# Performance work log

Measured on AMD Instinct MI355X. Metric: run time of the kernel, lower is better.

## Reference

```python
import jax, jax.numpy as jnp
import numpy as np

K = 3      # kernel size (hardcoded 3x3 in the torch module via repeat(...,9,...))
PAD = 1
STRIDE = 1


def _unfold(x):
    # torch.nn.functional.unfold equivalent: (B,C,H,W) -> (B,C,K,K,oh,ow)
    B, C, H, W = x.shape
    p = jax.lax.conv_general_dilated_patches(
        x, (K, K), (STRIDE, STRIDE), ((PAD, PAD), (PAD, PAD)))
    oh, ow = p.shape[2], p.shape[3]
    return p.reshape(B, C, K, K, oh, ow)


def setup_inputs() -> dict:
    key = jax.random.key(0)
    k1, k2, k3, k4 = jax.random.split(key, 4)
    B, Cin, Cout, H, W = 4, 64, 64, 128, 128
    inputs = jax.random.normal(k1, (B, Cin, H, W), jnp.float32)
    depth = jax.random.uniform(k2, (B, 1, H, W), jnp.float32)  # positive depths
    weight = jax.random.uniform(k3, (K, Cout, Cin, K, K), jnp.float32, minval=-0.05, maxval=0.05)
    bias = jax.random.uniform(k4, (Cout,), jnp.float32, minval=-0.05, maxval=0.05)
    return {"inputs": inputs, "depth": depth, "weight": weight, "bias": bias, "f": 1}


def reference(inputs, depth, weight, bias, f):
    # --- DepthKernelFn: per-depth-plane binary masks ---
    depth_wins = _unfold(depth)          # (B,1,K,K,oh,ow)
    s_wins = depth_wins / f              # grid spacing s_i = d / f
    cy, cx = K // 2, K // 2
    d0 = depth_wins[:, :, cy, cx]        # center depth      (B,1,oh,ow)
    s0 = s_wins[:, :, cy, cx]            # center spacing    (B,1,oh,ow)
    offs = jnp.arange(K, dtype=inputs.dtype) - (K - 1) / 2.0  # l - (K-1)/2
    # z_l at center: d0 + (l-1)*s0  -> (K,B,1,oh,ow)
    z0 = d0[None] + offs[:, None, None, None, None] * s0[None]
    half = s0[None] / 2
    a = (z0 - half)[:, :, :, None, None]  # (K,B,1,1,1,oh,ow)
    b = (z0 + half)[:, :, :, None, None]
    dw = depth_wins[None]                 # (1,B,1,K,K,oh,ow)
    # mask_l = 1 where a <= depth < b else 0  (same as the where-cascade in torch)
    mask = ((dw >= a) & (dw < b)).astype(inputs.dtype)  # (K,B,1,K,K,oh,ow)

    # --- RepeatKernelConvFn: masked windowed conv via einsum ---
    inp_wins = _unfold(inputs)            # (B,C,K,K,oh,ow)
    x = inp_wins[None] * mask             # (K,B,C,K,K,oh,ow), depth C=1 broadcasts
    out = jnp.einsum('hijklmn,hojkl->iomn', x, weight)
    out = out + bias.reshape(1, -1, 1, 1)
    return out
```

## Files before the change

kernel.cpp:

```cpp
#include <hip/hip_runtime.h>
#include <math.h>

#define B_N  4
#define CIN  64
#define COUT 64
#define H_N  128
#define W_N  128

typedef _Float16 half8 __attribute__((ext_vector_type(8)));
typedef float    f32x4 __attribute__((ext_vector_type(4)));

#define KTOT   1728
#define NSTEP  54
#define WA_BYTES ((size_t)NSTEP * 4 * 64 * 8 * 2)

__global__ void wprep(const float* __restrict__ w, _Float16* __restrict__ wa) {
    int idx = blockIdx.x * 256 + threadIdx.x;
    if (idx >= NSTEP * 4 * 64) return;
    int lane = idx & 63;
    int mt   = (idx >> 6) & 3;
    int s    = idx >> 8;
    int m    = mt * 16 + (lane & 15);
    int kl0  = (lane >> 4) * 8;
    _Float16 v[8];
#pragma unroll
    for (int j = 0; j < 8; ++j) {
        int k = s * 32 + kl0 + j;
        int g = k >> 6;
        int c = k & 63;
        int t = g / 3;
        int h = g % 3;
        v[j] = (_Float16)w[(((size_t)(h * COUT) + m) * CIN + c) * 9 + t];
    }
    *(int4*)&wa[(size_t)idx * 8] = *(int4*)v;
}

#define XS_STRIDE 72
#define XS_ROW    (130 * XS_STRIDE)

__global__ __launch_bounds__(256, 2)
void conv_mfma(const float* __restrict__ inp, const float* __restrict__ depth,
               const _Float16* __restrict__ wa, const float* __restrict__ bias,
               const int* __restrict__ fptr, float* __restrict__ out) {
    __shared__ _Float16 Xs[3 * XS_ROW];

    int bid  = blockIdx.x;
    int y    = bid & (H_N - 1);
    int b    = bid >> 7;
    int tid  = threadIdx.x;
    int lane = tid & 63;
    int wid  = tid >> 6;
    int mh   = wid & 1;
    int nh   = wid >> 1;
    int ln15 = lane & 15;
    int quad = lane >> 4;

    {
        int xl0 = tid & 63;
        int cq  = tid >> 6;
#pragma unroll
        for (int e = 0; e < 3; ++e) {
            int xl = e * 64 + xl0;
            if (e == 2 && xl0 >= 2) break;
            int gx = xl - 1;
            for (int dyi = 0; dyi < 3; ++dyi) {
                int yy = y + dyi - 1;
                _Float16 buf[16];
                if (yy >= 0 && yy < H_N && gx >= 0 && gx < W_N) {
                    const float* src = inp + (((size_t)b * CIN + cq * 16) * H_N + yy) * W_N + gx;
#pragma unroll
                    for (int cc = 0; cc < 16; ++cc)
                        buf[cc] = (_Float16)src[(size_t)cc * H_N * W_N];
                } else {
#pragma unroll
                    for (int cc = 0; cc < 16; ++cc) buf[cc] = (_Float16)0.f;
                }
                _Float16* dst = &Xs[dyi * XS_ROW + xl * XS_STRIDE + cq * 16];
                *(int4*)&dst[0] = *(int4*)&buf[0];
                *(int4*)&dst[8] = *(int4*)&buf[8];
            }
        }
    }

    double fd = (double)(*fptr);
    unsigned hpk[4];
#pragma unroll
    for (int nt = 0; nt < 4; ++nt) {
        int x = nh * 64 + nt * 16 + ln15;
        float d0f = depth[((size_t)b * H_N + y) * W_N + x];
        double dd = (double)d0f;
        double s0 = dd / fd;
        unsigned pk = 0;
        for (int t = 0; t < 9; ++t) {
            int dy = t / 3 - 1, dx = t % 3 - 1;
            int yy = y + dy, xx = x + dx;
            float dwf = (yy >= 0 && yy < H_N && xx >= 0 && xx < W_N)
                        ? depth[((size_t)b * H_N + yy) * W_N + xx] : 0.f;
            int h = -1;
            if (s0 > 0.0) {
                double u  = ((double)dwf - dd) / s0 + 1.5;
                double uf = floor(u);
                if (uf >= 0.0 && uf <= 2.0) h = (int)uf;
            }
            pk |= (unsigned)(h + 1) << (2 * t);
        }
        hpk[nt] = pk;
    }

    __syncthreads();

    f32x4 acc[2][4];
#pragma unroll
    for (int mt = 0; mt < 2; ++mt)
#pragma unroll
        for (int nt = 0; nt < 4; ++nt) acc[mt][nt] = (f32x4){0.f, 0.f, 0.f, 0.f};

    const half8* wa8 = (const half8*)wa;
    const half8 z = {(_Float16)0.f, (_Float16)0.f, (_Float16)0.f, (_Float16)0.f,
                     (_Float16)0.f, (_Float16)0.f, (_Float16)0.f, (_Float16)0.f};

    for (int t = 0; t < 9; ++t) {
        int dyi = t / 3;
        int dx  = t % 3 - 1;

        half8 A[6][2];
        {
            const half8* base = wa8 + ((size_t)t * 6 * 4 + mh * 2) * 64 + lane;
#pragma unroll
            for (int j = 0; j < 6; ++j)
#pragma unroll
                for (int mt = 0; mt < 2; ++mt)
                    A[j][mt] = base[(j * 4 + mt) * 64];
        }

        half8 braw[4][2];
#pragma unroll
        for (int nt = 0; nt < 4; ++nt) {
            int boff = dyi * XS_ROW + (nh * 64 + nt * 16 + ln15 + dx + 1) * XS_STRIDE + quad * 8;
            braw[nt][0] = *(const half8*)&Xs[boff];
            braw[nt][1] = *(const half8*)&Xs[boff + 32];
        }

#pragma unroll
        for (int h = 0; h < 3; ++h) {
#pragma unroll
            for (int nt = 0; nt < 4; ++nt) {
                bool m = (((hpk[nt] >> (2 * t)) & 3) == (unsigned)(h + 1));
#pragma unroll
                for (int kk = 0; kk < 2; ++kk) {
                    half8 bm = m ? braw[nt][kk] : z;
                    int j = h * 2 + kk;
#pragma unroll
                    for (int mt = 0; mt < 2; ++mt)
                        acc[mt][nt] = __builtin_amdgcn_mfma_f32_16x16x32_f16(A[j][mt], bm, acc[mt][nt], 0, 0, 0);
                }
            }
        }
    }

#pragma unroll
    for (int mt = 0; mt < 2; ++mt) {
#pragma unroll
        for (int nt = 0; nt < 4; ++nt) {
            int x = nh * 64 + nt * 16 + ln15;
#pragma unroll
            for (int r = 0; r < 4; ++r) {
                int o = mh * 32 + mt * 16 + quad * 4 + r;
                out[(((size_t)b * COUT + o) * H_N + y) * W_N + x] = acc[mt][nt][r] + bias[o];
            }
        }
    }
}

__global__ __launch_bounds__(256)
void conv25d(const float* __restrict__ inp, const float* __restrict__ depth,
             const float* __restrict__ wsrc, const float* __restrict__ bias,
             const int* __restrict__ fptr, float* __restrict__ out) {
    int bid = blockIdx.x;
    int xt  = bid & 3;
    int y   = (bid >> 2) & (H_N - 1);
    int b   = bid >> 9;
    int o   = threadIdx.x & 63;
    int q   = threadIdx.x >> 6;
    int x0  = xt * 32 + q * 8;
    double fd = (double)(*fptr);
    float acc[8];
    float bv = bias[o];
#pragma unroll
    for (int i = 0; i < 8; ++i) acc[i] = bv;
    const float* dcen = depth + ((size_t)b * H_N + y) * W_N;
    float d0[8];
#pragma unroll
    for (int i = 0; i < 8; ++i) d0[i] = dcen[x0 + i];
    for (int t = 0; t < 9; ++t) {
        int dy = t / 3 - 1, dx = t % 3 - 1;
        int yy = y + dy;
        if (yy < 0 || yy >= H_N) continue;
        const float* drow = depth + ((size_t)b * H_N + yy) * W_N;
        int hsel[8];
#pragma unroll
        for (int i = 0; i < 8; ++i) {
            int xx = x0 + i + dx;
            int h = -1;
            if (xx >= 0 && xx < W_N) {
                double dd = (double)d0[i];
                double s0 = dd / fd;
                if (s0 > 0.0) {
                    double u = ((double)drow[xx] - dd) / s0 + 1.5;
                    double uf = floor(u);
                    if (uf >= 0.0 && uf <= 2.0) h = (int)uf;
                }
            }
            hsel[i] = h;
        }
        const float* irow = inp + ((size_t)b * CIN * H_N + yy) * W_N;
        for (int c = 0; c < CIN; ++c) {
            const float* wb = wsrc + ((size_t)o * CIN + c) * 9 + t;
            float w0 = wb[0], w1 = wb[(size_t)COUT * CIN * 9], w2 = wb[2 * (size_t)COUT * CIN * 9];
            const float* ir = irow + (size_t)c * H_N * W_N;
#pragma unroll
            for (int i = 0; i < 8; ++i) {
                int h = hsel[i];
                if (h >= 0) {
                    float wv = (h == 0) ? w0 : ((h == 1) ? w1 : w2);
                    acc[i] = fmaf(ir[x0 + i + dx], wv, acc[i]);
                }
            }
        }
    }
    float* orow = out + (((size_t)b * COUT + o) * H_N + y) * W_N;
#pragma unroll
    for (int i = 0; i < 8; ++i) orow[x0 + i] = acc[i];
}

extern "C" void kernel_launch(void* const* d_in, const int* in_sizes, int n_in,
                              void* d_out, int out_size, void* d_ws, size_t ws_size,
                              hipStream_t stream) {
    const float* inp   = (const float*)d_in[0];
    const float* depth = (const float*)d_in[1];
    const float* w     = (const float*)d_in[2];
    const float* bias  = (const float*)d_in[3];
    const int*   f     = (const int*)d_in[4];
    float* out = (float*)d_out;

    if (ws_size >= WA_BYTES) {
        _Float16* wa = (_Float16*)d_ws;
        wprep<<<NSTEP, 256, 0, stream>>>(w, wa);
        conv_mfma<<<B_N * H_N, 256, 0, stream>>>(inp, depth, wa, bias, f, out);
    } else {
        conv25d<<<B_N * H_N * (W_N / 32), 256, 0, stream>>>(inp, depth, w, bias, f, out);
    }
}
```

Baseline: 108.3 us.

## Split rows into half-width blocks and stage weights via global_load_lds

Each block now covers half a row (64 pixels), which doubles the grid, and each wave owns 16 output channels instead of a 2x2 split. The input tile in LDS shrinks and occupancy hint rises to 3 blocks. Weight fragments are copied straight into LDS with global_load_lds instead of register loads, which cuts register pressure. The cost is more redundant input staging for the halo and more weight traffic, since the weights are now fetched per half-row.

```diff
diff --git a/kernel.cpp b/kernel.cpp
--- a/kernel.cpp
+++ b/kernel.cpp
@@ -13,6 +13,9 @@
 #define KTOT   1728
 #define NSTEP  54
 #define WA_BYTES ((size_t)NSTEP * 4 * 64 * 8 * 2)
+
+typedef const __attribute__((address_space(1))) void* gas_t;
+typedef __attribute__((address_space(3))) void* las_t;
 
 __global__ void wprep(const float* __restrict__ w, _Float16* __restrict__ wa) {
     int idx = blockIdx.x * 256 + threadIdx.x;
@@ -36,22 +39,23 @@
 }
 
 #define XS_STRIDE 72
-#define XS_ROW    (130 * XS_STRIDE)
-
-__global__ __launch_bounds__(256, 2)
+#define XS_ROW    (66 * XS_STRIDE)
+
+__global__ __launch_bounds__(256, 3)
 void conv_mfma(const float* __restrict__ inp, const float* __restrict__ depth,
                const _Float16* __restrict__ wa, const float* __restrict__ bias,
                const int* __restrict__ fptr, float* __restrict__ out) {
     __shared__ _Float16 Xs[3 * XS_ROW];
+    __shared__ _Float16 As[4 * 6 * 512];
 
     int bid  = blockIdx.x;
-    int y    = bid & (H_N - 1);
-    int b    = bid >> 7;
+    int xh   = bid & 1;
+    int y    = (bid >> 1) & (H_N - 1);
+    int b    = bid >> 8;
+    int x0   = xh * 64;
     int tid  = threadIdx.x;
     int lane = tid & 63;
     int wid  = tid >> 6;
-    int mh   = wid & 1;
-    int nh   = wid >> 1;
     int ln15 = lane & 15;
     int quad = lane >> 4;
 
@@ -59,10 +63,10 @@
         int xl0 = tid & 63;
         int cq  = tid >> 6;
 #pragma unroll
-        for (int e = 0; e < 3; ++e) {
-            int xl = e * 64 + xl0;
-            if (e == 2 && xl0 >= 2) break;
-            int gx = xl - 1;
+        for (int e = 0; e < 2; ++e) {
+            int xl = (e == 0) ? xl0 : 64 + xl0;
+            if (e == 1 && xl0 >= 2) break;
+            int gx = x0 - 1 + xl;
             for (int dyi = 0; dyi < 3; ++dyi) {
                 int yy = y + dyi - 1;
                 _Float16 buf[16];
@@ -86,7 +90,7 @@
     unsigned hpk[4];
 #pragma unroll
     for (int nt = 0; nt < 4; ++nt) {
-        int x = nh * 64 + nt * 16 + ln15;
+        int x = x0 + nt * 16 + ln15;
         float d0f = depth[((size_t)b * H_N + y) * W_N + x];
         double dd = (double)d0f;
         double s0 = dd / fd;
@@ -109,13 +113,10 @@
 
     __syncthreads();
 
-    f32x4 acc[2][4];
-#pragma unroll
-    for (int mt = 0; mt < 2; ++mt)
-#pragma unroll
-        for (int nt = 0; nt < 4; ++nt) acc[mt][nt] = (f32x4){0.f, 0.f, 0.f, 0.f};
-
-    const half8* wa8 = (const half8*)wa;
+    f32x4 acc[4];
+#pragma unroll
+    for (int nt = 0; nt < 4; ++nt) acc[nt] = (f32x4){0.f, 0.f, 0.f, 0.f};
+
     const half8 z = {(_Float16)0.f, (_Float16)0.f, (_Float16)0.f, (_Float16)0.f,
                      (_Float16)0.f, (_Float16)0.f, (_Float16)0.f, (_Float16)0.f};
 
@@ -123,51 +124,48 @@
         int dyi = t / 3;
         int dx  = t % 3 - 1;
 
-        half8 A[6][2];
-        {
-            const half8* base = wa8 + ((size_t)t * 6 * 4 + mh * 2) * 64 + lane;
-#pragma unroll
-            for (int j = 0; j < 6; ++j)
-#pragma unroll
-                for (int mt = 0; mt < 2; ++mt)
-                    A[j][mt] = base[(j * 4 + mt) * 64];
+#pragma unroll
+        for (int j = 0; j < 6; ++j) {
+            const _Float16* gsrc = wa + ((size_t)(((t * 6 + j) * 4 + wid) * 64) + lane) * 8;
+            __builtin_amdgcn_global_load_lds((gas_t)gsrc, (las_t)&As[(wid * 6 + j) * 512],
+                                             16, 0, 0);
         }
 
         half8 braw[4][2];
 #pragma unroll
         for (int nt = 0; nt < 4; ++nt) {
-            int boff = dyi * XS_ROW + (nh * 64 + nt * 16 + ln15 + dx + 1) * XS_STRIDE + quad * 8;
+            int boff = dyi * XS_ROW + (nt * 16 + ln15 + dx + 1) * XS_STRIDE + quad * 8;
             braw[nt][0] = *(const half8*)&Xs[boff];
             braw[nt][1] = *(const half8*)&Xs[boff + 32];
         }
 
-#pragma unroll
-        for (int h = 0; h < 3; ++h) {
+        unsigned hb[4];
+#pragma unroll
+        for (int nt = 0; nt < 4; ++nt) hb[nt] = (hpk[nt] >> (2 * t)) & 3;
+
+        __builtin_amdgcn_s_waitcnt(0x0F70);
+
+#pragma unroll
+        for (int j = 0; j < 6; ++j) {
+            half8 a = *(const half8*)&As[(wid * 6 + j) * 512 + lane * 8];
+            int h  = j >> 1;
+            int kk = j & 1;
 #pragma unroll
             for (int nt = 0; nt < 4; ++nt) {
-                bool m = (((hpk[nt] >> (2 * t)) & 3) == (unsigned)(h + 1));
-#pragma unroll
-                for (int kk = 0; kk < 2; ++kk) {
-                    half8 bm = m ? braw[nt][kk] : z;
-                    int j = h * 2 + kk;
-#pragma unroll
-                    for (int mt = 0; mt < 2; ++mt)
-                        acc[mt][nt] = __builtin_amdgcn_mfma_f32_16x16x32_f16(A[j][mt], bm, acc[mt][nt], 0, 0, 0);
-                }
-            }
-        }
-    }
-
-#pragma unroll
-    for (int mt = 0; mt < 2; ++mt) {
-#pragma unroll
-        for (int nt = 0; nt < 4; ++nt) {
-            int x = nh * 64 + nt * 16 + ln15;
-#pragma unroll
-            for (int r = 0; r < 4; ++r) {
-                int o = mh * 32 + mt * 16 + quad * 4 + r;
-                out[(((size_t)b * COUT + o) * H_N + y) * W_N + x] = acc[mt][nt][r] + bias[o];
-            }
+                bool m = (hb[nt] == (unsigned)(h + 1));
+                half8 bm = m ? braw[nt][kk] : z;
+                acc[nt] = __builtin_amdgcn_mfma_f32_16x16x32_f16(a, bm, acc[nt], 0, 0, 0);
+            }
+        }
+    }
+
+#pragma unroll
+    for (int nt = 0; nt < 4; ++nt) {
+        int x = x0 + nt * 16 + ln15;
+#pragma unroll
+        for (int r = 0; r < 4; ++r) {
+            int o = wid * 16 + quad * 4 + r;
+            out[(((size_t)b * COUT + o) * H_N + y) * W_N + x] = acc[nt][r] + bias[o];
         }
     }
 }
@@ -246,7 +244,7 @@
     if (ws_size >= WA_BYTES) {
         _Float16* wa = (_Float16*)d_ws;
         wprep<<<NSTEP, 256, 0, stream>>>(w, wa);
-        conv_mfma<<<B_N * H_N, 256, 0, stream>>>(inp, depth, wa, bias, f, out);
+        conv_mfma<<<B_N * H_N * 2, 256, 0, stream>>>(inp, depth, wa, bias, f, out);
     } else {
         conv25d<<<B_N * H_N * (W_N / 32), 256, 0, stream>>>(inp, depth, w, bias, f, out);
     }
```

Result: slower. 118.5 us (+9.5%).
